# Kernel tuning notes

Hardware: AMD Instinct MI355X
Metric: run time of the kernel (lower is better)

Reference implementation:

```python
import jax, jax.numpy as jnp
import numpy as np

N_EST = 5      # n_estimators
DEPTH = 6      # n_depth
LEAVES = 64    # 2 ** n_depth


def setup_inputs() -> dict:
    key = jax.random.key(0)
    ks = jax.random.split(key, 6)
    N, F, H, L, O = 131072, 256, 384, 64, 16
    X = jax.random.normal(ks[0], (N, F), jnp.float32)
    W1 = jax.random.normal(ks[1], (F, H), jnp.float32) / np.float32(np.sqrt(F))
    b1 = jnp.zeros((H,), jnp.float32)
    W2 = jax.random.normal(ks[2], (H, L), jnp.float32) / np.float32(np.sqrt(H))
    b2 = jnp.zeros((L,), jnp.float32)
    # phi[i] = random choice of n_leaves indices from arange(n_latent) without replacement
    phi = jnp.stack([jax.random.permutation(jax.random.fold_in(ks[3], i), L)[:LEAVES]
                     for i in range(N_EST)]).astype(jnp.int32)  # [E, 64]
    # pi: per-estimator leaf->label distributions (rows on the simplex, as after softmax updates)
    pi = jax.nn.softmax(jax.random.normal(ks[4], (N_EST, LEAVES, O), jnp.float32), axis=-1)
    return {"X": X, "W1": W1, "b1": b1, "W2": W2, "b2": b2, "phi": phi, "pi": pi}


def reference(X, W1, b1, W2, b2, phi, pi):
    # Backbone MLP: sigmoid -> sigmoid, as in keras.Sequential([Dense(h,'sigmoid'), Dense(l,'sigmoid')])
    h = jax.nn.sigmoid(X @ W1 + b1)          # [N, H]
    latent = jax.nn.sigmoid(h @ W2 + b2)     # [N, L]

    N = X.shape[0]
    E = phi.shape[0]
    d = latent[:, phi]                        # gather per estimator -> [N, E, 64]
    decisions = jnp.stack([d, 1.0 - d], axis=-1)  # [N, E, 64, 2] (go-left / go-right probs)

    # Soft tree routing: product of decision probs along each root->leaf path.
    # Level `lev` uses node indices [begin:begin+2**lev); index 0 is unused (matches TF code).
    mu = jnp.ones((N, E, 1, 1), X.dtype)
    begin = 1
    for lev in range(DEPTH):
        end = begin + 2 ** lev
        # reshape [N,E,k,2] -> [N,E,2k,1]; broadcast against [N,E,k_level,2] replaces tile(1,1,2)
        mu = mu.reshape(N, E, -1, 1) * decisions[:, :, begin:end, :]
        begin = end
    mu = mu.reshape(N, E, LEAVES)             # [N, E, 64] leaf arrival probabilities

    # predict: mean over estimators of mu_e @ pi_e
    return jnp.einsum('nel,elo->no', mu, pi) / E
```

## Files before the change

### kernel.cpp

```cpp
#include <hip/hip_runtime.h>
#include <hip/hip_bf16.h>
#include <stdint.h>

#define F_DIM 256
#define H_DIM 384
#define L_DIM 64
#define O_DIM 16
#define E_NUM 5
#define BM 32

#define XK_STRIDE 264
#define H_STRIDE 392
#define LAT_STRIDE 33
#define MU_STRIDE 328

typedef short bf16x8 __attribute__((ext_vector_type(8)));
typedef float f32x4 __attribute__((ext_vector_type(4)));

__device__ __forceinline__ unsigned short f2bf(float f) {
    union { float f; unsigned int u; } v; v.f = f;
    unsigned int u = v.u;
    return (unsigned short)((u + 0x7FFFu + ((u >> 16) & 1u)) >> 16);
}

__device__ __forceinline__ unsigned int pk2(float a, float b) {
#if defined(__has_builtin)
#if __has_builtin(__builtin_amdgcn_cvt_pk_bf16_f32)
    typedef __bf16 bf2 __attribute__((ext_vector_type(2)));
    bf2 p = __builtin_amdgcn_cvt_pk_bf16_f32(a, b);
    union { bf2 v; unsigned int u; } c; c.v = p;
    return c.u;
#else
    return (unsigned int)f2bf(a) | ((unsigned int)f2bf(b) << 16);
#endif
#else
    return (unsigned int)f2bf(a) | ((unsigned int)f2bf(b) << 16);
#endif
}

__device__ __forceinline__ uint2 cvt4(float4 v) {
    uint2 r; r.x = pk2(v.x, v.y); r.y = pk2(v.z, v.w); return r;
}

__device__ __forceinline__ float sigmoidf(float x) {
    return __builtin_amdgcn_rcpf(1.0f + __builtin_amdgcn_exp2f(-1.44269504088896f * x));
}

__global__ void prep_kernel(const float* __restrict__ W1, const float* __restrict__ W2,
                            const float* __restrict__ pi,
                            unsigned short* __restrict__ W1f,
                            unsigned short* __restrict__ W2f,
                            unsigned short* __restrict__ piTf) {
    __shared__ float tile[32][33];
    const int b = blockIdx.x;
    const int tid = threadIdx.x;
    const int tx = tid & 31, ty = tid >> 5;

    if (b < 120) {
        int ks, t0, nks;
        unsigned short* dst;
        if (b < 96) {
            const int fb = b / 12, hb = b % 12;
            #pragma unroll
            for (int s = 0; s < 32; s += 8)
                tile[ty + s][tx] = W1[(size_t)(fb * 32 + ty + s) * H_DIM + hb * 32 + tx];
            ks = fb; t0 = hb * 2; nks = 8; dst = W1f;
        } else {
            const int bb = b - 96, hb = bb / 2, lb = bb % 2;
            #pragma unroll
            for (int s = 0; s < 32; s += 8)
                tile[ty + s][tx] = W2[(size_t)(hb * 32 + ty + s) * L_DIM + lb * 32 + tx];
            ks = hb; t0 = lb * 2; nks = 12; dst = W2f;
        }
        __syncthreads();
        const int t_local = tid >> 7;
        const int r = (tid * 2) & 255;
        const int lane = r >> 2;
        const int e2b = r & 3;
        const int q = lane >> 4, c = lane & 15;
        const int f0 = q * 8 + e2b * 2;
        const int hl = t_local * 16 + c;
        uint2 v;
        v.x = pk2(tile[f0 + 0][hl], tile[f0 + 1][hl]);
        v.y = pk2(tile[f0 + 2][hl], tile[f0 + 3][hl]);
        const size_t off = ((size_t)((t0 + t_local) * nks + ks) * 64 + lane) * 8 + e2b * 2;
        *(uint2*)(dst + off) = v;
    } else {
        for (int i = tid; i < O_DIM * E_NUM * L_DIM; i += 256) {
            const int j = i & 7, lane = (i >> 3) & 63, ks = i >> 9;
            const int q = lane >> 4, c = lane & 15;
            const int k = ks * 32 + q * 8 + j;
            piTf[i] = f2bf(pi[k * O_DIM + c] * 0.2f);
        }
    }
}

__global__ __launch_bounds__(256, 3) void fused_kernel(
    const float* __restrict__ X,
    const unsigned short* __restrict__ W1f,
    const float* __restrict__ b1,
    const unsigned short* __restrict__ W2f,
    const float* __restrict__ b2,
    const int* __restrict__ phi,
    const unsigned short* __restrict__ piTf,
    float* __restrict__ out) {

    __shared__ __align__(16) unsigned char smem[34816];
    unsigned short* Xs  = (unsigned short*)smem;
    unsigned short* Hs  = (unsigned short*)smem;
    float*          latT = (float*)(smem + 25088);
    int*            phis = (int*)(smem + 33536);
    unsigned short* mus = (unsigned short*)smem;

    const int tid  = threadIdx.x;
    const int wave = tid >> 6;
    const int lane = tid & 63;
    const int q    = lane >> 4;
    const int c    = lane & 15;
    const int row0 = blockIdx.x * BM;

    for (int idx = tid; idx < E_NUM * L_DIM; idx += 256) phis[idx] = phi[idx];

    #pragma unroll
    for (int h = 0; h < 2; ++h) {
        float4 t0[4];
        #pragma unroll
        for (int i = 0; i < 4; ++i)
            t0[i] = *(const float4*)(X + (size_t)(row0 + wave * 8 + h * 4 + i) * F_DIM + lane * 4);
        #pragma unroll
        for (int i = 0; i < 4; ++i)
            *(uint2*)&Xs[(wave * 8 + h * 4 + i) * XK_STRIDE + lane * 4] = cvt4(t0[i]);
    }

    bf16x8 af0[6];
    #pragma unroll
    for (int i = 0; i < 6; ++i)
        af0[i] = *(const bf16x8*)(W1f + ((size_t)(wave * 48 + i * 8 + 0) * 64 + lane) * 8);

    __syncthreads();

    f32x4 acc[6][2];
    #pragma unroll
    for (int i = 0; i < 6; ++i)
        #pragma unroll
        for (int j = 0; j < 2; ++j)
            acc[i][j] = (f32x4){0.f, 0.f, 0.f, 0.f};

    {
        bf16x8 bf0[2];
        #pragma unroll
        for (int j = 0; j < 2; ++j)
            bf0[j] = *(const bf16x8*)&Xs[(j * 16 + c) * XK_STRIDE + q * 8];
        #pragma unroll
        for (int i = 0; i < 6; ++i)
            #pragma unroll
            for (int j = 0; j < 2; ++j)
                acc[i][j] = __builtin_amdgcn_mfma_f32_16x16x32_bf16(af0[i], bf0[j], acc[i][j], 0, 0, 0);
    }
    #pragma unroll 2
    for (int ks = 1; ks < 8; ++ks) {
        bf16x8 af[6];
        #pragma unroll
        for (int i = 0; i < 6; ++i)
            af[i] = *(const bf16x8*)(W1f + ((size_t)(wave * 48 + i * 8 + ks) * 64 + lane) * 8);
        bf16x8 bf_[2];
        #pragma unroll
        for (int j = 0; j < 2; ++j)
            bf_[j] = *(const bf16x8*)&Xs[(j * 16 + c) * XK_STRIDE + ks * 32 + q * 8];
        #pragma unroll
        for (int i = 0; i < 6; ++i)
            #pragma unroll
            for (int j = 0; j < 2; ++j)
                acc[i][j] = __builtin_amdgcn_mfma_f32_16x16x32_bf16(af[i], bf_[j], acc[i][j], 0, 0, 0);
    }
    __syncthreads();

    const int nbase = wave * 96;
    #pragma unroll
    for (int i = 0; i < 6; ++i) {
        const int n0 = nbase + i * 16 + q * 4;
        float4 bv = *(const float4*)(b1 + n0);
        #pragma unroll
        for (int j = 0; j < 2; ++j) {
            const int m = j * 16 + c;
            uint2 h2;
            h2.x = pk2(sigmoidf(acc[i][j][0] + bv.x), sigmoidf(acc[i][j][1] + bv.y));
            h2.y = pk2(sigmoidf(acc[i][j][2] + bv.z), sigmoidf(acc[i][j][3] + bv.w));
            *(uint2*)&Hs[m * H_STRIDE + n0] = h2;
        }
    }
    __syncthreads();

    {
        bf16x8 wfrag[12];
        #pragma unroll
        for (int ks = 0; ks < 12; ++ks)
            wfrag[ks] = *(const bf16x8*)(W2f + ((size_t)(wave * 12 + ks) * 64 + lane) * 8);
        f32x4 acc2[2];
        acc2[0] = (f32x4){0.f, 0.f, 0.f, 0.f};
        acc2[1] = (f32x4){0.f, 0.f, 0.f, 0.f};
        #pragma unroll
        for (int ks = 0; ks < 12; ++ks) {
            #pragma unroll
            for (int j = 0; j < 2; ++j) {
                bf16x8 bf_ = *(const bf16x8*)&Hs[(j * 16 + c) * H_STRIDE + ks * 32 + q * 8];
                acc2[j] = __builtin_amdgcn_mfma_f32_16x16x32_bf16(wfrag[ks], bf_, acc2[j], 0, 0, 0);
            }
        }
        const int lb = wave * 16;
        const float4 b2v = *(const float4*)(b2 + lb + q * 4);
        #pragma unroll
        for (int j = 0; j < 2; ++j) {
            const int m = j * 16 + c;
            #pragma unroll
            for (int rg = 0; rg < 4; ++rg) {
                const int l = lb + q * 4 + rg;
                latT[l * LAT_STRIDE + m] = sigmoidf(acc2[j][rg] + ((const float*)&b2v)[rg]);
            }
        }
    }
    __syncthreads();

    {
        const int r = lane & 31;
        const int e = wave * 2 + (lane >> 5);
        if (e < E_NUM) {
            float mu[64];
            mu[0] = 1.0f;
            #pragma unroll
            for (int lev = 0; lev < 6; ++lev) {
                const int w = 1 << lev;
                #pragma unroll
                for (int i = w - 1; i >= 0; --i) {
                    float d = latT[phis[e * 64 + w + i] * LAT_STRIDE + r];
                    float m = mu[i];
                    mu[2 * i + 1] = m - m * d;
                    mu[2 * i]     = m * d;
                }
            }
            #pragma unroll
            for (int j8 = 0; j8 < 8; ++j8) {
                bf16x8 v;
                #pragma unroll
                for (int t = 0; t < 4; ++t) {
                    unsigned int p = pk2(mu[j8 * 8 + 2 * t], mu[j8 * 8 + 2 * t + 1]);
                    v[2 * t]     = (short)(p & 0xFFFF);
                    v[2 * t + 1] = (short)(p >> 16);
                }
                *((bf16x8*)&mus[r * MU_STRIDE + e * 64 + j8 * 8]) = v;
            }
        }
    }
    __syncthreads();

    if (wave < 2) {
        const int mt = wave;
        bf16x8 pfrag[10];
        #pragma unroll
        for (int ks = 0; ks < 10; ++ks)
            pfrag[ks] = *(const bf16x8*)(piTf + ((size_t)ks * 64 + lane) * 8);
        f32x4 acc3 = (f32x4){0.f, 0.f, 0.f, 0.f};
        #pragma unroll
        for (int ks = 0; ks < 10; ++ks) {
            bf16x8 af = *((const bf16x8*)&mus[(mt * 16 + c) * MU_STRIDE + ks * 32 + q * 8]);
            acc3 = __builtin_amdgcn_mfma_f32_16x16x32_bf16(af, pfrag[ks], acc3, 0, 0, 0);
        }
        #pragma unroll
        for (int rg = 0; rg < 4; ++rg) {
            const int m = mt * 16 + q * 4 + rg;
            out[(size_t)(row0 + m) * O_DIM + c] = acc3[rg];
        }
    }
}

extern "C" void kernel_launch(void* const* d_in, const int* in_sizes, int n_in,
                              void* d_out, int out_size, void* d_ws, size_t ws_size,
                              hipStream_t stream) {
    (void)in_sizes; (void)n_in; (void)out_size; (void)ws_size;
    const float* X  = (const float*)d_in[0];
    const float* W1 = (const float*)d_in[1];
    const float* b1 = (const float*)d_in[2];
    const float* W2 = (const float*)d_in[3];
    const float* b2 = (const float*)d_in[4];
    const int*   phi = (const int*)d_in[5];
    const float* pi  = (const float*)d_in[6];
    float* out = (float*)d_out;

    unsigned short* W1f  = (unsigned short*)d_ws;
    unsigned short* W2f  = (unsigned short*)((char*)d_ws + 196608);
    unsigned short* piTf = (unsigned short*)((char*)d_ws + 196608 + 49152);

    prep_kernel<<<121, 256, 0, stream>>>(W1, W2, pi, W1f, W2f, piTf);

    const int nblocks = 131072 / BM;
    fused_kernel<<<nblocks, 256, 0, stream>>>(X, W1f, b1, W2f, b2, phi, piTf, out);
}
```

Baseline: 248.7 us.

## Make fused kernel persistent over four row tiles with register-prefetched X

Each block now processes four 32-row tiles in a loop, prefetching the next tile's X rows into registers while the current tile's epilogue, second GEMM and tree routing run. It also folds the bias into the sigmoid exponent with an FMA, rewrites the tree routing as a nested depth-first product that avoids a 64-entry register array, and raises the launch-bounds occupancy hint from 3 to 4 blocks per CU. The aim is to hide global-load latency for X and cut per-block setup cost. In exchange there are four times fewer blocks, extra per-tile barriers, and more register pressure from the prefetch buffer under a tighter occupancy target.

```diff
diff --git a/kernel.cpp b/kernel.cpp
--- a/kernel.cpp
+++ b/kernel.cpp
@@ -8,6 +8,7 @@
 #define O_DIM 16
 #define E_NUM 5
 #define BM 32
+#define T_TILES 4
 
 #define XK_STRIDE 264
 #define H_STRIDE 392
@@ -42,8 +43,9 @@
     uint2 r; r.x = pk2(v.x, v.y); r.y = pk2(v.z, v.w); return r;
 }
 
-__device__ __forceinline__ float sigmoidf(float x) {
-    return __builtin_amdgcn_rcpf(1.0f + __builtin_amdgcn_exp2f(-1.44269504088896f * x));
+#define KLOG2E (-1.44269504088896f)
+__device__ __forceinline__ float sig2(float a, float kb) {
+    return __builtin_amdgcn_rcpf(1.0f + __builtin_amdgcn_exp2f(fmaf(a, KLOG2E, kb)));
 }
 
 __global__ void prep_kernel(const float* __restrict__ W1, const float* __restrict__ W2,
@@ -95,7 +97,7 @@
     }
 }
 
-__global__ __launch_bounds__(256, 3) void fused_kernel(
+__global__ __launch_bounds__(256, 4) void fused_kernel(
     const float* __restrict__ X,
     const unsigned short* __restrict__ W1f,
     const float* __restrict__ b1,
@@ -117,159 +119,168 @@
     const int lane = tid & 63;
     const int q    = lane >> 4;
     const int c    = lane & 15;
-    const int row0 = blockIdx.x * BM;
+    const int blockRow0 = blockIdx.x * (BM * T_TILES);
 
     for (int idx = tid; idx < E_NUM * L_DIM; idx += 256) phis[idx] = phi[idx];
 
+    float4 f4[8];
     #pragma unroll
-    for (int h = 0; h < 2; ++h) {
-        float4 t0[4];
+    for (int i = 0; i < 8; ++i)
+        f4[i] = *(const float4*)(X + (size_t)(blockRow0 + wave * 8 + i) * F_DIM + lane * 4);
+
+    for (int it = 0; it < T_TILES; ++it) {
+        const int row0 = blockRow0 + it * BM;
+
         #pragma unroll
-        for (int i = 0; i < 4; ++i)
-            t0[i] = *(const float4*)(X + (size_t)(row0 + wave * 8 + h * 4 + i) * F_DIM + lane * 4);
-        #pragma unroll
-        for (int i = 0; i < 4; ++i)
-            *(uint2*)&Xs[(wave * 8 + h * 4 + i) * XK_STRIDE + lane * 4] = cvt4(t0[i]);
-    }
-
-    bf16x8 af0[6];
-    #pragma unroll
-    for (int i = 0; i < 6; ++i)
-        af0[i] = *(const bf16x8*)(W1f + ((size_t)(wave * 48 + i * 8 + 0) * 64 + lane) * 8);
-
-    __syncthreads();
-
-    f32x4 acc[6][2];
-    #pragma unroll
-    for (int i = 0; i < 6; ++i)
-        #pragma unroll
-        for (int j = 0; j < 2; ++j)
-            acc[i][j] = (f32x4){0.f, 0.f, 0.f, 0.f};
-
-    {
-        bf16x8 bf0[2];
-        #pragma unroll
-        for (int j = 0; j < 2; ++j)
-            bf0[j] = *(const bf16x8*)&Xs[(j * 16 + c) * XK_STRIDE + q * 8];
+        for (int i = 0; i < 8; ++i)
+            *(uint2*)&Xs[(wave * 8 + i) * XK_STRIDE + lane * 4] = cvt4(f4[i]);
+
+        __syncthreads();
+
+        f32x4 acc[6][2];
         #pragma unroll
         for (int i = 0; i < 6; ++i)
             #pragma unroll
             for (int j = 0; j < 2; ++j)
-                acc[i][j] = __builtin_amdgcn_mfma_f32_16x16x32_bf16(af0[i], bf0[j], acc[i][j], 0, 0, 0);
-    }
-    #pragma unroll 2
-    for (int ks = 1; ks < 8; ++ks) {
-        bf16x8 af[6];
+                acc[i][j] = (f32x4){0.f, 0.f, 0.f, 0.f};
+
+        #pragma unroll 2
+        for (int ks = 0; ks < 8; ++ks) {
+            bf16x8 af[6];
+            #pragma unroll
+            for (int i = 0; i < 6; ++i)
+                af[i] = *(const bf16x8*)(W1f + ((size_t)(wave * 48 + i * 8 + ks) * 64 + lane) * 8);
+            bf16x8 bf_[2];
+            #pragma unroll
+            for (int j = 0; j < 2; ++j)
+                bf_[j] = *(const bf16x8*)&Xs[(j * 16 + c) * XK_STRIDE + ks * 32 + q * 8];
+            #pragma unroll
+            for (int i = 0; i < 6; ++i)
+                #pragma unroll
+                for (int j = 0; j < 2; ++j)
+                    acc[i][j] = __builtin_amdgcn_mfma_f32_16x16x32_bf16(af[i], bf_[j], acc[i][j], 0, 0, 0);
+        }
+        __syncthreads();
+
+        if (it < T_TILES - 1) {
+            const int nrow0 = blockRow0 + (it + 1) * BM;
+            #pragma unroll
+            for (int i = 0; i < 8; ++i)
+                f4[i] = *(const float4*)(X + (size_t)(nrow0 + wave * 8 + i) * F_DIM + lane * 4);
+        }
+
+        const int nbase = wave * 96;
         #pragma unroll
-        for (int i = 0; i < 6; ++i)
-            af[i] = *(const bf16x8*)(W1f + ((size_t)(wave * 48 + i * 8 + ks) * 64 + lane) * 8);
-        bf16x8 bf_[2];
-        #pragma unroll
-        for (int j = 0; j < 2; ++j)
-            bf_[j] = *(const bf16x8*)&Xs[(j * 16 + c) * XK_STRIDE + ks * 32 + q * 8];
-        #pragma unroll
-        for (int i = 0; i < 6; ++i)
-            #pragma unroll
-            for (int j = 0; j < 2; ++j)
-                acc[i][j] = __builtin_amdgcn_mfma_f32_16x16x32_bf16(af[i], bf_[j], acc[i][j], 0, 0, 0);
-    }
-    __syncthreads();
-
-    const int nbase = wave * 96;
-    #pragma unroll
-    for (int i = 0; i < 6; ++i) {
-        const int n0 = nbase + i * 16 + q * 4;
-        float4 bv = *(const float4*)(b1 + n0);
-        #pragma unroll
-        for (int j = 0; j < 2; ++j) {
-            const int m = j * 16 + c;
-            uint2 h2;
-            h2.x = pk2(sigmoidf(acc[i][j][0] + bv.x), sigmoidf(acc[i][j][1] + bv.y));
-            h2.y = pk2(sigmoidf(acc[i][j][2] + bv.z), sigmoidf(acc[i][j][3] + bv.w));
-            *(uint2*)&Hs[m * H_STRIDE + n0] = h2;
-        }
-    }
-    __syncthreads();
-
-    {
-        bf16x8 wfrag[12];
-        #pragma unroll
-        for (int ks = 0; ks < 12; ++ks)
-            wfrag[ks] = *(const bf16x8*)(W2f + ((size_t)(wave * 12 + ks) * 64 + lane) * 8);
-        f32x4 acc2[2];
-        acc2[0] = (f32x4){0.f, 0.f, 0.f, 0.f};
-        acc2[1] = (f32x4){0.f, 0.f, 0.f, 0.f};
-        #pragma unroll
-        for (int ks = 0; ks < 12; ++ks) {
+        for (int i = 0; i < 6; ++i) {
+            const int n0 = nbase + i * 16 + q * 4;
+            float4 bv = *(const float4*)(b1 + n0);
+            const float kb0 = KLOG2E * bv.x, kb1 = KLOG2E * bv.y;
+            const float kb2 = KLOG2E * bv.z, kb3 = KLOG2E * bv.w;
             #pragma unroll
             for (int j = 0; j < 2; ++j) {
-                bf16x8 bf_ = *(const bf16x8*)&Hs[(j * 16 + c) * H_STRIDE + ks * 32 + q * 8];
-                acc2[j] = __builtin_amdgcn_mfma_f32_16x16x32_bf16(wfrag[ks], bf_, acc2[j], 0, 0, 0);
-            }
-        }
-        const int lb = wave * 16;
-        const float4 b2v = *(const float4*)(b2 + lb + q * 4);
-        #pragma unroll
-        for (int j = 0; j < 2; ++j) {
-            const int m = j * 16 + c;
+                const int m = j * 16 + c;
+                uint2 h2;
+                h2.x = pk2(sig2(acc[i][j][0], kb0), sig2(acc[i][j][1], kb1));
+                h2.y = pk2(sig2(acc[i][j][2], kb2), sig2(acc[i][j][3], kb3));
+                *(uint2*)&Hs[m * H_STRIDE + n0] = h2;
+            }
+        }
+        __syncthreads();
+
+        {
+            bf16x8 wfrag[12];
+            #pragma unroll
+            for (int ks = 0; ks < 12; ++ks)
+                wfrag[ks] = *(const bf16x8*)(W2f + ((size_t)(wave * 12 + ks) * 64 + lane) * 8);
+            f32x4 acc2[2];
+            acc2[0] = (f32x4){0.f, 0.f, 0.f, 0.f};
+            acc2[1] = (f32x4){0.f, 0.f, 0.f, 0.f};
+            #pragma unroll
+            for (int ks = 0; ks < 12; ++ks) {
+                #pragma unroll
+                for (int j = 0; j < 2; ++j) {
+                    bf16x8 bf_ = *(const bf16x8*)&Hs[(j * 16 + c) * H_STRIDE + ks * 32 + q * 8];
+                    acc2[j] = __builtin_amdgcn_mfma_f32_16x16x32_bf16(wfrag[ks], bf_, acc2[j], 0, 0, 0);
+                }
+            }
+            const int lb = wave * 16;
+            const float4 b2v = *(const float4*)(b2 + lb + q * 4);
+            const float kb0 = KLOG2E * b2v.x, kb1 = KLOG2E * b2v.y;
+            const float kb2 = KLOG2E * b2v.z, kb3 = KLOG2E * b2v.w;
+            #pragma unroll
+            for (int j = 0; j < 2; ++j) {
+                const int m = j * 16 + c;
+                const int l0 = lb + q * 4;
+                latT[(l0 + 0) * LAT_STRIDE + m] = sig2(acc2[j][0], kb0);
+                latT[(l0 + 1) * LAT_STRIDE + m] = sig2(acc2[j][1], kb1);
+                latT[(l0 + 2) * LAT_STRIDE + m] = sig2(acc2[j][2], kb2);
+                latT[(l0 + 3) * LAT_STRIDE + m] = sig2(acc2[j][3], kb3);
+            }
+        }
+        __syncthreads();
+
+        {
+            const int r = lane & 31;
+            const int e = wave * 2 + (lane >> 5);
+            if (e < E_NUM) {
+                const int base = e * 64;
+                const float d0 = latT[phis[base + 1] * LAT_STRIDE + r];
+                #pragma unroll
+                for (int b0 = 0; b0 < 2; ++b0) {
+                    const float p1 = b0 ? (1.0f - d0) : d0;
+                    const float d1 = latT[phis[base + 2 + b0] * LAT_STRIDE + r];
+                    #pragma unroll
+                    for (int b1 = 0; b1 < 2; ++b1) {
+                        const int i2 = b0 * 2 + b1;
+                        const float p2 = p1 * (b1 ? (1.0f - d1) : d1);
+                        const float d2 = latT[phis[base + 4 + i2] * LAT_STRIDE + r];
+                        #pragma unroll
+                        for (int b2 = 0; b2 < 2; ++b2) {
+                            const int i3 = i2 * 2 + b2;
+                            const float p3 = p2 * (b2 ? (1.0f - d2) : d2);
+                            const float d3 = latT[phis[base + 8 + i3] * LAT_STRIDE + r];
+                            #pragma unroll
+                            for (int b3 = 0; b3 < 2; ++b3) {
+                                const int i4 = i3 * 2 + b3;
+                                const float p4 = p3 * (b3 ? (1.0f - d3) : d3);
+                                const float d4 = latT[phis[base + 16 + i4] * LAT_STRIDE + r];
+                                uint2 w2;
+                                #pragma unroll
+                                for (int b4 = 0; b4 < 2; ++b4) {
+                                    const int i5 = i4 * 2 + b4;
+                                    const float p5 = p4 * (b4 ? (1.0f - d4) : d4);
+                                    const float d5 = latT[phis[base + 32 + i5] * LAT_STRIDE + r];
+                                    const unsigned int w = pk2(p5 * d5, p5 * (1.0f - d5));
+                                    if (b4 == 0) w2.x = w; else w2.y = w;
+                                }
+                                *(uint2*)&mus[r * MU_STRIDE + e * 64 + i4 * 4] = w2;
+                            }
+                        }
+                    }
+                }
+            }
+        }
+        __syncthreads();
+
+        if (wave < 2) {
+            const int mt = wave;
+            bf16x8 pfrag[10];
+            #pragma unroll
+            for (int ks = 0; ks < 10; ++ks)
+                pfrag[ks] = *(const bf16x8*)(piTf + ((size_t)ks * 64 + lane) * 8);
+            f32x4 acc3 = (f32x4){0.f, 0.f, 0.f, 0.f};
+            #pragma unroll
+            for (int ks = 0; ks < 10; ++ks) {
+                bf16x8 af = *((const bf16x8*)&mus[(mt * 16 + c) * MU_STRIDE + ks * 32 + q * 8]);
+                acc3 = __builtin_amdgcn_mfma_f32_16x16x32_bf16(af, pfrag[ks], acc3, 0, 0, 0);
+            }
             #pragma unroll
             for (int rg = 0; rg < 4; ++rg) {
-                const int l = lb + q * 4 + rg;
-                latT[l * LAT_STRIDE + m] = sigmoidf(acc2[j][rg] + ((const float*)&b2v)[rg]);
-            }
-        }
-    }
-    __syncthreads();
-
-    {
-        const int r = lane & 31;
-        const int e = wave * 2 + (lane >> 5);
-        if (e < E_NUM) {
-            float mu[64];
-            mu[0] = 1.0f;
-            #pragma unroll
-            for (int lev = 0; lev < 6; ++lev) {
-                const int w = 1 << lev;
-                #pragma unroll
-                for (int i = w - 1; i >= 0; --i) {
-                    float d = latT[phis[e * 64 + w + i] * LAT_STRIDE + r];
-                    float m = mu[i];
-                    mu[2 * i + 1] = m - m * d;
-                    mu[2 * i]     = m * d;
-                }
-            }
-            #pragma unroll
-            for (int j8 = 0; j8 < 8; ++j8) {
-                bf16x8 v;
-                #pragma unroll
-                for (int t = 0; t < 4; ++t) {
-                    unsigned int p = pk2(mu[j8 * 8 + 2 * t], mu[j8 * 8 + 2 * t + 1]);
-                    v[2 * t]     = (short)(p & 0xFFFF);
-                    v[2 * t + 1] = (short)(p >> 16);
-                }
-                *((bf16x8*)&mus[r * MU_STRIDE + e * 64 + j8 * 8]) = v;
-            }
-        }
-    }
-    __syncthreads();
-
-    if (wave < 2) {
-        const int mt = wave;
-        bf16x8 pfrag[10];
-        #pragma unroll
-        for (int ks = 0; ks < 10; ++ks)
-            pfrag[ks] = *(const bf16x8*)(piTf + ((size_t)ks * 64 + lane) * 8);
-        f32x4 acc3 = (f32x4){0.f, 0.f, 0.f, 0.f};
-        #pragma unroll
-        for (int ks = 0; ks < 10; ++ks) {
-            bf16x8 af = *((const bf16x8*)&mus[(mt * 16 + c) * MU_STRIDE + ks * 32 + q * 8]);
-            acc3 = __builtin_amdgcn_mfma_f32_16x16x32_bf16(af, pfrag[ks], acc3, 0, 0, 0);
-        }
-        #pragma unroll
-        for (int rg = 0; rg < 4; ++rg) {
-            const int m = mt * 16 + q * 4 + rg;
-            out[(size_t)(row0 + m) * O_DIM + c] = acc3[rg];
-        }
+                const int m = mt * 16 + q * 4 + rg;
+                out[(size_t)(row0 + m) * O_DIM + c] = acc3[rg];
+            }
+        }
+        __syncthreads();
     }
 }
 
@@ -292,6 +303,6 @@
 
     prep_kernel<<<121, 256, 0, stream>>>(W1, W2, pi, W1f, W2f, piTf);
 
-    const int nblocks = 131072 / BM;
+    const int nblocks = 131072 / (BM * T_TILES);
     fused_kernel<<<nblocks, 256, 0, stream>>>(X, W1f, b1, W2f, b2, phi, piTf, out);
 }
```

New measurement: 312.4 us. +25.6%, slower.
